# Kernel tuning notes

Measured on AMD Instinct MI355X. Metric: run time of the kernel, lower is better.

The kernel has to match this reference:

```python
import jax, jax.numpy as jnp
import numpy as np

NUM_HEADS = 12
HEAD_DIM = 64
HIDDEN = 768
QMAX = 127.0  # 8-bit symmetric
DOMAIN_MIN, DOMAIN_MAX = -10.0, 0.0
NUM_INTERVALS = 12


def _build_pla_coeffs():
    xs = np.linspace(DOMAIN_MIN, DOMAIN_MAX, 1001)
    ys = np.exp(xs)
    intervals = np.linspace(DOMAIN_MIN, DOMAIN_MAX, NUM_INTERVALS + 1)
    ms, cs = [], []
    for i in range(NUM_INTERVALS):
        a, b = intervals[i], intervals[i + 1]
        mask = (xs >= a) & (xs <= b)
        m, c = np.polyfit(xs[mask], ys[mask], 1)
        ms.append(m)
        cs.append(c)
    return (jnp.asarray(ms, jnp.float32), jnp.asarray(cs, jnp.float32),
            jnp.asarray(intervals, jnp.float32))

COEFFS_M, COEFFS_C, INTERVALS = _build_pla_coeffs()


def quantize(x):
    # per-row (last-dim) abs-max symmetric 8-bit fake quant
    max_val = jnp.max(jnp.abs(x), axis=-1, keepdims=True)
    scale = max_val / QMAX
    scale = jnp.where(scale == 0, 1.0, scale)
    return jnp.clip(jnp.round(x / scale), -QMAX, QMAX) * scale


def to_fixed_point(x, bits=32, frac_bits=26):
    scale = 2.0 ** frac_bits
    lo = -2.0 ** (bits - 1)
    hi = 2.0 ** (bits - 1) - 1
    return jnp.clip(jnp.round(x * scale), lo, hi) / scale


def pla_exp(x):
    xc = jnp.clip(x, DOMAIN_MIN, DOMAIN_MAX)
    # sum(x >= intervals) - 1 == searchsorted(intervals, x, 'right') - 1
    idx = jnp.clip(jnp.searchsorted(INTERVALS, xc, side='right') - 1, 0, NUM_INTERVALS - 1)
    return COEFFS_M[idx] * xc + COEFFS_C[idx]


def pla_softmax(scores):
    shifted = scores - jnp.max(scores, axis=-1, keepdims=True)
    shifted_fx = to_fixed_point(shifted, 32, 26)
    exps = pla_exp(shifted_fx)
    sm = exps / (jnp.sum(exps, axis=-1, keepdims=True) + 1e-9)
    return quantize(sm)


def q_linear(x, W, b):
    # QuantizedLinear: quantize input and weight (per-row), fp bias
    return quantize(x) @ quantize(W).T + b


def split_heads(x):
    B, S, _ = x.shape
    return x.reshape(B, S, NUM_HEADS, HEAD_DIM).transpose(0, 2, 1, 3)  # bhsd


def mhsa(hidden_states, Wq, bq, Wk, bk, Wv, bv, Wo, bo):
    B, S, H = hidden_states.shape
    scale = HEAD_DIM ** -0.5
    q = split_heads(q_linear(hidden_states, Wq, bq))
    k = split_heads(q_linear(hidden_states, Wk, bk))
    v = split_heads(q_linear(hidden_states, Wv, bv))
    # per-row quantization makes tile-wise quant identical to full quant
    scores = jnp.einsum('bhqd,bhkd->bhqk', quantize(q), quantize(k)) * scale
    probs = pla_softmax(scores)
    ctx = jnp.einsum('bhqk,bhkd->bhqd', probs, quantize(v))
    ctx = ctx.transpose(0, 2, 1, 3).reshape(B, S, H)
    return q_linear(ctx, Wo, bo)


def setup_inputs() -> dict:
    key = jax.random.key(0)
    ks = jax.random.split(key, 9)
    B, S = 8, 512
    hs = jax.random.normal(ks[0], (B, S, HIDDEN), dtype=jnp.float32)
    def w(k):
        return jax.random.normal(k, (HIDDEN, HIDDEN), dtype=jnp.float32) * 0.02
    def b(k):
        return jax.random.normal(k, (HIDDEN,), dtype=jnp.float32) * 0.02
    return {
        'hidden_states': hs,
        'Wq': w(ks[1]), 'bq': b(ks[2]),
        'Wk': w(ks[3]), 'bk': b(ks[4]),
        'Wv': w(ks[5]), 'bv': b(ks[6]),
        'Wo': w(ks[7]), 'bo': b(ks[8]),
    }


def reference(hidden_states, Wq, bq, Wk, bk, Wv, bv, Wo, bo):
    return mhsa(hidden_states, Wq, bq, Wk, bk, Wv, bv, Wo, bo)
```

## Files before the change

### kernel.cpp

```cpp
#include <hip/hip_runtime.h>
#include <cmath>

#define R_TOT 4096
#define HID   768
#define NHEAD 12
#define HDIM  64
#define SEQ   512
#define BATCH 8

typedef int   v4i  __attribute__((ext_vector_type(4)));
typedef float v4f  __attribute__((ext_vector_type(4)));
typedef _Float16 half8 __attribute__((ext_vector_type(8)));
typedef _Float16 half4v __attribute__((ext_vector_type(4)));

__device__ __forceinline__ void gl_lds16(const signed char* g, signed char* l) {
  __builtin_amdgcn_global_load_lds(
      (const __attribute__((address_space(1))) void*)g,
      (__attribute__((address_space(3))) void*)l, 16, 0, 0);
}

struct PlaConsts { float m[12]; float c[12]; float b[13]; };

static PlaConsts build_pla() {
  PlaConsts pc;
  const int NPTS = 1001;
  static double xs[NPTS], ys[NPTS];
  const double step = 10.0 / 1000.0;
  for (int j = 0; j < NPTS; ++j) xs[j] = (double)j * step + (-10.0);
  xs[NPTS - 1] = 0.0;
  for (int j = 0; j < NPTS; ++j) ys[j] = std::exp(xs[j]);
  double bnd[13];
  const double step2 = 10.0 / 12.0;
  for (int k = 0; k < 13; ++k) bnd[k] = (double)k * step2 + (-10.0);
  bnd[12] = 0.0;
  for (int i = 0; i < 12; ++i) {
    const double a = bnd[i], bb = bnd[i + 1];
    double sx = 0, sy = 0; int n = 0;
    for (int j = 0; j < NPTS; ++j)
      if (xs[j] >= a && xs[j] <= bb) { sx += xs[j]; sy += ys[j]; ++n; }
    const double xm = sx / n, ym = sy / n;
    double sxx = 0, sxy = 0;
    for (int j = 0; j < NPTS; ++j)
      if (xs[j] >= a && xs[j] <= bb) {
        const double dx = xs[j] - xm;
        sxx += dx * dx; sxy += dx * (ys[j] - ym);
      }
    const double m = sxy / sxx;
    pc.m[i] = (float)m;
    pc.c[i] = (float)(ym - m * xm);
  }
  for (int k = 0; k < 13; ++k) pc.b[k] = (float)bnd[k];
  return pc;
}
static const PlaConsts g_pla = build_pla();

__device__ __forceinline__ void quant_row_wave(const float* __restrict__ x,
                                               signed char* __restrict__ qrow,
                                               float* __restrict__ srow) {
  const int lane = threadIdx.x & 63;
  const float4* x4 = (const float4*)x;
  const float4 a = x4[lane];
  const float4 b = x4[lane + 64];
  const float4 c = x4[lane + 128];
  float m = fmaxf(fmaxf(fabsf(a.x), fabsf(a.y)), fmaxf(fabsf(a.z), fabsf(a.w)));
  m = fmaxf(m, fmaxf(fmaxf(fabsf(b.x), fabsf(b.y)), fmaxf(fabsf(b.z), fabsf(b.w))));
  m = fmaxf(m, fmaxf(fmaxf(fabsf(c.x), fabsf(c.y)), fmaxf(fabsf(c.z), fabsf(c.w))));
  #pragma unroll
  for (int off = 32; off; off >>= 1) m = fmaxf(m, __shfl_xor(m, off));
  float s = m / 127.0f;
  if (s == 0.f) s = 1.f;
  auto qb = [&](float v) -> int {
    return ((int)fminf(fmaxf(rintf(v / s), -127.f), 127.f)) & 255;
  };
  const int p0 = qb(a.x) | (qb(a.y) << 8) | (qb(a.z) << 16) | (qb(a.w) << 24);
  const int p1 = qb(b.x) | (qb(b.y) << 8) | (qb(b.z) << 16) | (qb(b.w) << 24);
  const int p2 = qb(c.x) | (qb(c.y) << 8) | (qb(c.z) << 16) | (qb(c.w) << 24);
  int* q4 = (int*)qrow;
  q4[lane] = p0;
  q4[lane + 64] = p1;
  q4[lane + 128] = p2;
  if (lane == 0) *srow = s;
}

__global__ __launch_bounds__(256)
void quant_rows(const float* __restrict__ src,
                signed char* __restrict__ qout, float* __restrict__ sout) {
  const int row = blockIdx.x * 4 + (threadIdx.x >> 6);
  quant_row_wave(src + (size_t)row * HID, qout + (size_t)row * HID, sout + row);
}

__global__ __launch_bounds__(256)
void quant_all(const float* hs, const float* w0, const float* w1,
               const float* w2, const float* w3,
               signed char* qx, float* sx,
               signed char* q0, signed char* q1, signed char* q2, signed char* q3,
               float* s0, float* s1, float* s2, float* s3) {
  const int row = blockIdx.x * 4 + (threadIdx.x >> 6);
  const float* src; signed char* qo; float* so; int r;
  if (row < R_TOT)             { src = hs; qo = qx; so = sx; r = row; }
  else if (row < R_TOT + 768)  { src = w0; qo = q0; so = s0; r = row - R_TOT; }
  else if (row < R_TOT + 1536) { src = w1; qo = q1; so = s1; r = row - R_TOT - 768; }
  else if (row < R_TOT + 2304) { src = w2; qo = q2; so = s2; r = row - R_TOT - 1536; }
  else                         { src = w3; qo = q3; so = s3; r = row - R_TOT - 2304; }
  quant_row_wave(src + (size_t)r * HID, qo + (size_t)r * HID, so + r);
}

__device__ __forceinline__
void proj_stage(const signed char* __restrict__ qx,
                const signed char* __restrict__ qw,
                int row0, int col0, int k0,
                signed char* __restrict__ Ab, signed char* __restrict__ Bb,
                int w, int lr, int cg) {
  #pragma unroll
  for (int m = 0; m < 4; ++m) {
    const int ci = w * 4 + m;
    gl_lds16(qx + (size_t)(row0 + ci * 8 + lr) * HID + k0 + cg * 16,
             Ab + ci * 1024);
  }
  #pragma unroll
  for (int m = 0; m < 2; ++m) {
    const int ci = w * 2 + m;
    gl_lds16(qw + (size_t)(col0 + ci * 8 + lr) * HID + k0 + cg * 16,
             Bb + ci * 1024);
  }
}

__device__ __forceinline__
void proj_body(int mode,
               const signed char* __restrict__ qx, const float* __restrict__ sx,
               const signed char* __restrict__ qw, const float* __restrict__ sw,
               const float* __restrict__ bias,
               signed char* __restrict__ qo, float* __restrict__ so,
               _Float16* __restrict__ vt, float* __restrict__ fo,
               signed char* Al, signed char* Bl) {
  const int tid = threadIdx.x;
  const int w = tid >> 6, lane = tid & 63;
  const int n = lane & 15, quad = lane >> 4;
  const int row0 = blockIdx.x * 128, col0 = blockIdx.y * 64;
  const int lr = lane >> 3;
  const int lc = lane & 7;
  const int cg = lc ^ lr;
  v4i acc[2][4];
  #pragma unroll
  for (int s = 0; s < 2; ++s)
    #pragma unroll
    for (int j = 0; j < 4; ++j) acc[s][j] = (v4i){0, 0, 0, 0};

  proj_stage(qx, qw, row0, col0, 0, Al, Bl, w, lr, cg);
  __syncthreads();

  #pragma unroll
  for (int it = 0; it < 6; ++it) {
    signed char* Ac = Al + (it & 1) * 16384;
    signed char* Bc = Bl + (it & 1) * 8192;
    if (it < 5)
      proj_stage(qx, qw, row0, col0, (it + 1) * 128,
                 Al + ((it & 1) ^ 1) * 16384, Bl + ((it & 1) ^ 1) * 8192,
                 w, lr, cg);
    #pragma unroll
    for (int ks4 = 0; ks4 < 8; ks4 += 4) {
      const int sw16 = ((quad + ks4) ^ (n & 7)) * 16;
      const v4i af0 = *(const v4i*)&Ac[(w * 16 + n) * 128 + sw16];
      const v4i af1 = *(const v4i*)&Ac[(64 + w * 16 + n) * 128 + sw16];
      #pragma unroll
      for (int j = 0; j < 4; ++j) {
        const v4i bf = *(const v4i*)&Bc[(j * 16 + n) * 128 + sw16];
        acc[0][j] = __builtin_amdgcn_mfma_i32_16x16x64_i8(af0, bf, acc[0][j], 0, 0, 0);
        acc[1][j] = __builtin_amdgcn_mfma_i32_16x16x64_i8(af1, bf, acc[1][j], 0, 0, 0);
      }
    }
    if (it < 5) __syncthreads();
  }

  float swc4[4], bc4[4];
  #pragma unroll
  for (int j = 0; j < 4; ++j) {
    swc4[j] = sw[col0 + j * 16 + n];
    bc4[j] = bias[col0 + j * 16 + n];
  }
  #pragma unroll
  for (int s = 0; s < 2; ++s) {
    const int mrow = s * 64 + w * 16 + quad * 4;
    float sxr[4];
    #pragma unroll
    for (int r = 0; r < 4; ++r) sxr[r] = sx[row0 + mrow + r];
    float vals[4][4];
    #pragma unroll
    for (int j = 0; j < 4; ++j)
      #pragma unroll
      for (int r = 0; r < 4; ++r)
        vals[j][r] = (float)acc[s][j][r] * (sxr[r] * swc4[j]) + bc4[j];
    if (mode == 1) {
      const int h = blockIdx.y;
      #pragma unroll
      for (int r = 0; r < 4; ++r) {
        float m = 0.f;
        #pragma unroll
        for (int j = 0; j < 4; ++j) m = fmaxf(m, fabsf(vals[j][r]));
        #pragma unroll
        for (int off = 1; off < 16; off <<= 1) m = fmaxf(m, __shfl_xor(m, off));
        float sq = m / 127.0f;
        if (sq == 0.f) sq = 1.f;
        const int grow = row0 + mrow + r;
        const int bidx = grow >> 9, sidx = grow & 511;
        const size_t rowidx = ((size_t)bidx * NHEAD + h) * SEQ + sidx;
        #pragma unroll
        for (int j = 0; j < 4; ++j) {
          float q = fminf(fmaxf(rintf(vals[j][r] / sq), -127.f), 127.f);
          qo[rowidx * HDIM + j * 16 + n] = (signed char)(int)q;
        }
        if (n == 0) so[rowidx] = sq;
      }
    } else if (mode == 2) {
      const int h = blockIdx.y;
      float srow[4];
      #pragma unroll
      for (int r = 0; r < 4; ++r) {
        float m = 0.f;
        #pragma unroll
        for (int j = 0; j < 4; ++j) m = fmaxf(m, fabsf(vals[j][r]));
        #pragma unroll
        for (int off = 1; off < 16; off <<= 1) m = fmaxf(m, __shfl_xor(m, off));
        float sq = m / 127.0f;
        if (sq == 0.f) sq = 1.f;
        srow[r] = sq;
      }
      const int grow0 = row0 + mrow;
      const int bidx = grow0 >> 9, sidx = grow0 & 511;
      const int kb = sidx >> 5, ko = sidx & 31;
      const size_t hbv = (size_t)bidx * NHEAD + h;
      #pragma unroll
      for (int j = 0; j < 4; ++j) {
        half4v hv;
        #pragma unroll
        for (int r = 0; r < 4; ++r) {
          float q = fminf(fmaxf(rintf(vals[j][r] / srow[r]), -127.f), 127.f);
          hv[r] = (_Float16)(q * srow[r]);
        }
        *(half4v*)(vt + ((hbv * 16 + kb) * 64 + j * 16 + n) * 32 + ko) = hv;
      }
    } else {
      #pragma unroll
      for (int r = 0; r < 4; ++r) {
        const size_t base = (size_t)(row0 + mrow + r) * HID + col0;
        #pragma unroll
        for (int j = 0; j < 4; ++j)
          fo[base + j * 16 + n] = vals[j][r];
      }
    }
  }
}

__global__ __launch_bounds__(256)
void proj_qkv(const signed char* __restrict__ qx, const float* __restrict__ sx,
              const signed char* qwq, const float* swq, const float* bq,
              signed char* qqd, float* qqs,
              const signed char* qwk, const float* swk, const float* bk,
              signed char* qkd, float* qks,
              const signed char* qwv, const float* swv, const float* bv,
              _Float16* vt2) {
  __shared__ __align__(16) signed char Al[2 * 128 * 128];
  __shared__ __align__(16) signed char Bl[2 * 64 * 128];
  if (blockIdx.z == 0)
    proj_body(1, qx, sx, qwq, swq, bq, qqd, qqs, nullptr, nullptr, Al, Bl);
  else if (blockIdx.z == 1)
    proj_body(1, qx, sx, qwk, swk, bk, qkd, qks, nullptr, nullptr, Al, Bl);
  else
    proj_body(2, qx, sx, qwv, swv, bv, nullptr, nullptr, vt2, nullptr, Al, Bl);
}

__global__ __launch_bounds__(256)
void proj_out(const signed char* __restrict__ qx, const float* __restrict__ sx,
              const signed char* qw, const float* sw, const float* bias,
              float* fo) {
  __shared__ __align__(16) signed char Al[2 * 128 * 128];
  __shared__ __align__(16) signed char Bl[2 * 64 * 128];
  proj_body(0, qx, sx, qw, sw, bias, nullptr, nullptr, nullptr, fo, Al, Bl);
}

__device__ __forceinline__
void softmax_exp_tile(float (&s)[8][4], float mx26, const float4* __restrict__ pt4,
                      float& sum_out, float& amax_out) {
  float sum = 0.f, amax = 0.f;
  #pragma unroll
  for (int t = 0; t < 8; ++t) {
    #pragma unroll
    for (int r = 0; r < 4; ++r) {
      float sh = s[t][r] - mx26;
      sh = fmaxf(sh, -671088640.0f);
      const float tq = rintf(sh);
      const float xc = tq * 1.4901161193847656e-08f;
      int g = (int)((xc + 10.0f) * 1.2f);
      g = g > 11 ? 11 : g;
      float4 E = pt4[g];
      int gn = g + ((xc >= E.y) ? 1 : 0) - ((xc < E.x) ? 1 : 0);
      gn = gn < 0 ? 0 : (gn > 11 ? 11 : gn);
      if (gn != g) E = pt4[gn];
      const float e = __fadd_rn(__fmul_rn(E.z, xc), E.w);
      s[t][r] = e;
      sum += e;
      amax = fmaxf(amax, fabsf(e));
    }
  }
  sum += __shfl_xor(sum, 16);
  sum += __shfl_xor(sum, 32);
  amax = fmaxf(amax, __shfl_xor(amax, 16));
  amax = fmaxf(amax, __shfl_xor(amax, 32));
  sum_out = sum; amax_out = amax;
}

__device__ __forceinline__
void quant_pack_tile(const float (&s)[8][4], float t127,
                     _Float16* __restrict__ phtrow, int w, int quad) {
  #pragma unroll
  for (int t = 0; t < 8; ++t) {
    half4v hq;
    #pragma unroll
    for (int r = 0; r < 4; ++r) {
      const float qf = fminf(fmaxf(rintf(s[t][r] * t127), -127.f), 127.f);
      hq[r] = (_Float16)qf;
    }
    *(half4v*)&phtrow[(t * 4 + w) * 16 + quad * 4] = hq;
  }
}

__device__ __forceinline__
v4f pv_tile(const _Float16* __restrict__ vbase, const _Float16* __restrict__ prow) {
  v4f acc = {0.f, 0.f, 0.f, 0.f};
  #pragma unroll
  for (int kt = 0; kt < 16; ++kt) {
    const half8 bf = *(const half8*)(vbase + kt * 2048);
    acc = __builtin_amdgcn_mfma_f32_16x16x32_f16(*(const half8*)(prow + kt * 32), bf, acc, 0, 0, 0);
  }
  return acc;
}

#define PSTR 520
__global__ __launch_bounds__(256)
void attn_kernel(const signed char* __restrict__ qq, const float* __restrict__ qss,
                 const signed char* __restrict__ qk, const float* __restrict__ kss,
                 const _Float16* __restrict__ vt2,
                 float* __restrict__ ctx, const PlaConsts pc) {
  __shared__ __align__(16) _Float16 PhT[2][16 * PSTR];
  __shared__ __align__(16) float red_max[2][16][4];
  __shared__ __align__(16) float red_sum[2][16][4];
  __shared__ __align__(16) float red_amax[2][16][4];
  __shared__ float psa[2][16];
  __shared__ __align__(16) float4 pt4[12];

  const int tid = threadIdx.x;
  const int q0 = blockIdx.x * 32;
  const int hh = blockIdx.y, bz = blockIdx.z;
  const size_t hb = (size_t)bz * NHEAD + hh;
  const signed char* qqh = qq + (hb * SEQ + q0) * HDIM;
  const signed char* qkh = qk + hb * SEQ * HDIM;
  const float* ksp = kss + hb * SEQ;

  if (tid < 12)
    pt4[tid] = make_float4(pc.b[tid], pc.b[tid + 1], pc.m[tid], pc.c[tid]);

  const int w = tid >> 6, lane = tid & 63;
  const int n = lane & 15, quad = lane >> 4;

  float s26[2][8][4];
  {
    const v4i qf0 = *(const v4i*)(qqh + (size_t)n * HDIM + quad * 16);
    const v4i qf1 = *(const v4i*)(qqh + (size_t)(16 + n) * HDIM + quad * 16);
    const float qs0 = (qss[hb * SEQ + q0 + n] * 0.125f) * 67108864.0f;
    const float qs1 = (qss[hb * SEQ + q0 + 16 + n] * 0.125f) * 67108864.0f;
    float vmax0 = -3.0e38f, vmax1 = -3.0e38f;
    #pragma unroll
    for (int t = 0; t < 8; ++t) {
      const int kc0 = (t * 4 + w) * 16;
      const v4i kfrag = *(const v4i*)(qkh + (size_t)(kc0 + n) * HDIM + quad * 16);
      const float4 ks4 = *(const float4*)(ksp + kc0 + quad * 4);
      v4i zero = {};
      const v4i a0 = __builtin_amdgcn_mfma_i32_16x16x64_i8(kfrag, qf0, zero, 0, 0, 0);
      const v4i a1 = __builtin_amdgcn_mfma_i32_16x16x64_i8(kfrag, qf1, zero, 0, 0, 0);
      const float ks[4] = {ks4.x, ks4.y, ks4.z, ks4.w};
      #pragma unroll
      for (int r = 0; r < 4; ++r) {
        const float v0 = (float)a0[r] * (qs0 * ks[r]);
        const float v1 = (float)a1[r] * (qs1 * ks[r]);
        s26[0][t][r] = v0; vmax0 = fmaxf(vmax0, v0);
        s26[1][t][r] = v1; vmax1 = fmaxf(vmax1, v1);
      }
    }
    vmax0 = fmaxf(vmax0, __shfl_xor(vmax0, 16));
    vmax0 = fmaxf(vmax0, __shfl_xor(vmax0, 32));
    vmax1 = fmaxf(vmax1, __shfl_xor(vmax1, 16));
    vmax1 = fmaxf(vmax1, __shfl_xor(vmax1, 32));
    if (quad == 0) { red_max[0][n][w] = vmax0; red_max[1][n][w] = vmax1; }
  }
  __syncthreads();

  {
    const float4 rm = *(const float4*)&red_max[0][n][0];
    const float mx26 = fmaxf(fmaxf(rm.x, rm.y), fmaxf(rm.z, rm.w));
    float sum, amax;
    softmax_exp_tile(s26[0], mx26, pt4, sum, amax);
    if (quad == 0) { red_sum[0][n][w] = sum; red_amax[0][n][w] = amax; }
  }
  __syncthreads();

  {
    const float4 rs = *(const float4*)&red_sum[0][n][0];
    const float4 ra = *(const float4*)&red_amax[0][n][0];
    float denom = (rs.x + rs.y) + (rs.z + rs.w);
    denom = __fadd_rn(denom, 1e-9f);
    const float rden = 1.0f / denom;
    const float am = fmaxf(fmaxf(ra.x, ra.y), fmaxf(ra.z, ra.w));
    float ps = (am * rden) / 127.0f;
    if (ps == 0.f) ps = 1.f;
    if (w == 0 && quad == 0) psa[0][n] = ps;
    const float t127 = 127.0f / am;
    quant_pack_tile(s26[0], t127, &PhT[0][n * PSTR], w, quad);

    const float4 rm = *(const float4*)&red_max[1][n][0];
    const float mx26 = fmaxf(fmaxf(rm.x, rm.y), fmaxf(rm.z, rm.w));
    float sum, amax;
    softmax_exp_tile(s26[1], mx26, pt4, sum, amax);
    if (quad == 0) { red_sum[1][n][w] = sum; red_amax[1][n][w] = amax; }
  }
  __syncthreads();

  const _Float16* vbase = vt2 + ((size_t)hb * 16 * 64 + (w * 16 + n)) * 32 + quad * 8;

  {
    const v4f acc0 = pv_tile(vbase, &PhT[0][n * PSTR + quad * 8]);

    const float4 rs = *(const float4*)&red_sum[1][n][0];
    const float4 ra = *(const float4*)&red_amax[1][n][0];
    float denom = (rs.x + rs.y) + (rs.z + rs.w);
    denom = __fadd_rn(denom, 1e-9f);
    const float rden = 1.0f / denom;
    const float am = fmaxf(fmaxf(ra.x, ra.y), fmaxf(ra.z, ra.w));
    float ps = (am * rden) / 127.0f;
    if (ps == 0.f) ps = 1.f;
    if (w == 0 && quad == 0) psa[1][n] = ps;
    const float t127 = 127.0f / am;
    quant_pack_tile(s26[1], t127, &PhT[1][n * PSTR], w, quad);

    #pragma unroll
    for (int r = 0; r < 4; ++r) {
      const int row = quad * 4 + r;
      ctx[((size_t)bz * SEQ + q0 + row) * HID + (size_t)hh * HDIM + w * 16 + n] =
          acc0[r] * psa[0][row];
    }
  }
  __syncthreads();

  {
    const v4f acc1 = pv_tile(vbase, &PhT[1][n * PSTR + quad * 8]);
    #pragma unroll
    for (int r = 0; r < 4; ++r) {
      const int row = quad * 4 + r;
      ctx[((size_t)bz * SEQ + q0 + 16 + row) * HID + (size_t)hh * HDIM + w * 16 + n] =
          acc1[r] * psa[1][row];
    }
  }
}

extern "C" void kernel_launch(void* const* d_in, const int* in_sizes, int n_in,
                              void* d_out, int out_size, void* d_ws, size_t ws_size,
                              hipStream_t stream) {
  (void)in_sizes; (void)n_in; (void)out_size; (void)ws_size;
  const float* hs = (const float*)d_in[0];
  const float* Wq = (const float*)d_in[1];
  const float* bq = (const float*)d_in[2];
  const float* Wk = (const float*)d_in[3];
  const float* bk = (const float*)d_in[4];
  const float* Wv = (const float*)d_in[5];
  const float* bv = (const float*)d_in[6];
  const float* Wo = (const float*)d_in[7];
  const float* bo = (const float*)d_in[8];
  float* out = (float*)d_out;

  char* ws = (char*)d_ws;
  size_t off = 0;
  auto alloc = [&](size_t bytes) -> char* {
    char* p = ws + off;
    off += (bytes + 255) & ~(size_t)255;
    return p;
  };
  signed char* qx  = (signed char*)alloc((size_t)R_TOT * HID);
  float*       sx  = (float*)alloc((size_t)R_TOT * 4);
  signed char* qwq = (signed char*)alloc((size_t)HID * HID);
  signed char* qwk = (signed char*)alloc((size_t)HID * HID);
  signed char* qwv = (signed char*)alloc((size_t)HID * HID);
  signed char* qwo = (signed char*)alloc((size_t)HID * HID);
  float*       swq = (float*)alloc((size_t)HID * 4);
  float*       swk = (float*)alloc((size_t)HID * 4);
  float*       swv = (float*)alloc((size_t)HID * 4);
  float*       swo = (float*)alloc((size_t)HID * 4);
  signed char* qqd = (signed char*)alloc((size_t)R_TOT * HID);
  float*       qqs = (float*)alloc((size_t)BATCH * NHEAD * SEQ * 4);
  signed char* qkd = (signed char*)alloc((size_t)R_TOT * HID);
  float*       qks = (float*)alloc((size_t)BATCH * NHEAD * SEQ * 4);
  float*       ctx = (float*)alloc((size_t)R_TOT * HID * 4);
  _Float16*    vt2 = (_Float16*)alloc((size_t)BATCH * NHEAD * HDIM * SEQ * 2);
  signed char* qc  = qx;
  float*       scs = sx;

  quant_all<<<(R_TOT + 4 * HID) / 4, 256, 0, stream>>>(
      hs, Wq, Wk, Wv, Wo, qx, sx,
      qwq, qwk, qwv, qwo, swq, swk, swv, swo);

  proj_qkv<<<dim3(R_TOT / 128, HID / 64, 3), 256, 0, stream>>>(
      qx, sx, qwq, swq, bq, qqd, qqs,
      qwk, swk, bk, qkd, qks,
      qwv, swv, bv, vt2);

  attn_kernel<<<dim3(SEQ / 32, NHEAD, BATCH), 256, 0, stream>>>(
      qqd, qqs, qkd, qks, vt2, ctx, g_pla);

  quant_rows<<<R_TOT / 4, 256, 0, stream>>>(ctx, qc, scs);
  proj_out<<<dim3(R_TOT / 128, HID / 64), 256, 0, stream>>>(
      qc, scs, qwo, swo, bo, out);
}
```

Before: 152.0 us.

## Fuse all pipeline stages into one cooperative persistent kernel with grid syncs

Replaces the five separate kernel launches with one cooperative persistent kernel of 768 blocks. Each stage loops over its former grid's work items and stages are separated by grid-wide barriers, with shared memory reused across stages. This removes launch gaps and per-kernel ramp-up and tail between stages. In exchange it adds grid.sync cost, fixes occupancy at 3 blocks per CU with a 48KB shared buffer, and leaves load imbalance where a stage's work count is not a multiple of the grid size. The old multi-launch path is kept as a fallback if the cooperative launch fails.

```diff
diff --git a/kernel.cpp b/kernel.cpp
--- a/kernel.cpp
+++ b/kernel.cpp
@@ -1,5 +1,8 @@
 #include <hip/hip_runtime.h>
+#include <hip/hip_cooperative_groups.h>
 #include <cmath>
+
+namespace cg = cooperative_groups;
 
 #define R_TOT 4096
 #define HID   768
@@ -7,6 +10,7 @@
 #define HDIM  64
 #define SEQ   512
 #define BATCH 8
+#define GRID_N 768
 
 typedef int   v4i  __attribute__((ext_vector_type(4)));
 typedef float v4f  __attribute__((ext_vector_type(4)));
@@ -82,6 +86,22 @@
   if (lane == 0) *srow = s;
 }
 
+__device__ __forceinline__
+void quant_all_job(int row, const float* hs, const float* w0, const float* w1,
+                   const float* w2, const float* w3,
+                   signed char* qx, float* sx,
+                   signed char* q0, signed char* q1, signed char* q2,
+                   signed char* q3,
+                   float* s0, float* s1, float* s2, float* s3) {
+  const float* src; signed char* qo; float* so; int r;
+  if (row < R_TOT)             { src = hs; qo = qx; so = sx; r = row; }
+  else if (row < R_TOT + 768)  { src = w0; qo = q0; so = s0; r = row - R_TOT; }
+  else if (row < R_TOT + 1536) { src = w1; qo = q1; so = s1; r = row - R_TOT - 768; }
+  else if (row < R_TOT + 2304) { src = w2; qo = q2; so = s2; r = row - R_TOT - 1536; }
+  else                         { src = w3; qo = q3; so = s3; r = row - R_TOT - 2304; }
+  quant_row_wave(src + (size_t)r * HID, qo + (size_t)r * HID, so + r);
+}
+
 __global__ __launch_bounds__(256)
 void quant_rows(const float* __restrict__ src,
                 signed char* __restrict__ qout, float* __restrict__ sout) {
@@ -96,13 +116,7 @@
                signed char* q0, signed char* q1, signed char* q2, signed char* q3,
                float* s0, float* s1, float* s2, float* s3) {
   const int row = blockIdx.x * 4 + (threadIdx.x >> 6);
-  const float* src; signed char* qo; float* so; int r;
-  if (row < R_TOT)             { src = hs; qo = qx; so = sx; r = row; }
-  else if (row < R_TOT + 768)  { src = w0; qo = q0; so = s0; r = row - R_TOT; }
-  else if (row < R_TOT + 1536) { src = w1; qo = q1; so = s1; r = row - R_TOT - 768; }
-  else if (row < R_TOT + 2304) { src = w2; qo = q2; so = s2; r = row - R_TOT - 1536; }
-  else                         { src = w3; qo = q3; so = s3; r = row - R_TOT - 2304; }
-  quant_row_wave(src + (size_t)r * HID, qo + (size_t)r * HID, so + r);
+  quant_all_job(row, hs, w0, w1, w2, w3, qx, sx, q0, q1, q2, q3, s0, s1, s2, s3);
 }
 
 __device__ __forceinline__
@@ -126,7 +140,7 @@
 }
 
 __device__ __forceinline__
-void proj_body(int mode,
+void proj_body(int mode, int bx, int by,
                const signed char* __restrict__ qx, const float* __restrict__ sx,
                const signed char* __restrict__ qw, const float* __restrict__ sw,
                const float* __restrict__ bias,
@@ -136,7 +150,7 @@
   const int tid = threadIdx.x;
   const int w = tid >> 6, lane = tid & 63;
   const int n = lane & 15, quad = lane >> 4;
-  const int row0 = blockIdx.x * 128, col0 = blockIdx.y * 64;
+  const int row0 = bx * 128, col0 = by * 64;
   const int lr = lane >> 3;
   const int lc = lane & 7;
   const int cg = lc ^ lr;
@@ -146,6 +160,7 @@
     #pragma unroll
     for (int j = 0; j < 4; ++j) acc[s][j] = (v4i){0, 0, 0, 0};
 
+  __syncthreads();
   proj_stage(qx, qw, row0, col0, 0, Al, Bl, w, lr, cg);
   __syncthreads();
 
@@ -191,7 +206,7 @@
       for (int r = 0; r < 4; ++r)
         vals[j][r] = (float)acc[s][j][r] * (sxr[r] * swc4[j]) + bc4[j];
     if (mode == 1) {
-      const int h = blockIdx.y;
+      const int h = by;
       #pragma unroll
       for (int r = 0; r < 4; ++r) {
         float m = 0.f;
@@ -212,7 +227,7 @@
         if (n == 0) so[rowidx] = sq;
       }
     } else if (mode == 2) {
-      const int h = blockIdx.y;
+      const int h = by;
       float srow[4];
       #pragma unroll
       for (int r = 0; r < 4; ++r) {
@@ -262,11 +277,11 @@
   __shared__ __align__(16) signed char Al[2 * 128 * 128];
   __shared__ __align__(16) signed char Bl[2 * 64 * 128];
   if (blockIdx.z == 0)
-    proj_body(1, qx, sx, qwq, swq, bq, qqd, qqs, nullptr, nullptr, Al, Bl);
+    proj_body(1, blockIdx.x, blockIdx.y, qx, sx, qwq, swq, bq, qqd, qqs, nullptr, nullptr, Al, Bl);
   else if (blockIdx.z == 1)
-    proj_body(1, qx, sx, qwk, swk, bk, qkd, qks, nullptr, nullptr, Al, Bl);
+    proj_body(1, blockIdx.x, blockIdx.y, qx, sx, qwk, swk, bk, qkd, qks, nullptr, nullptr, Al, Bl);
   else
-    proj_body(2, qx, sx, qwv, swv, bv, nullptr, nullptr, vt2, nullptr, Al, Bl);
+    proj_body(2, blockIdx.x, blockIdx.y, qx, sx, qwv, swv, bv, nullptr, nullptr, vt2, nullptr, Al, Bl);
 }
 
 __global__ __launch_bounds__(256)
@@ -275,7 +290,7 @@
               float* fo) {
   __shared__ __align__(16) signed char Al[2 * 128 * 128];
   __shared__ __align__(16) signed char Bl[2 * 64 * 128];
-  proj_body(0, qx, sx, qw, sw, bias, nullptr, nullptr, nullptr, fo, Al, Bl);
+  proj_body(0, blockIdx.x, blockIdx.y, qx, sx, qw, sw, bias, nullptr, nullptr, nullptr, fo, Al, Bl);
 }
 
 __device__ __forceinline__
@@ -336,28 +351,21 @@
 }
 
 #define PSTR 520
-__global__ __launch_bounds__(256)
-void attn_kernel(const signed char* __restrict__ qq, const float* __restrict__ qss,
-                 const signed char* __restrict__ qk, const float* __restrict__ kss,
-                 const _Float16* __restrict__ vt2,
-                 float* __restrict__ ctx, const PlaConsts pc) {
-  __shared__ __align__(16) _Float16 PhT[2][16 * PSTR];
-  __shared__ __align__(16) float red_max[2][16][4];
-  __shared__ __align__(16) float red_sum[2][16][4];
-  __shared__ __align__(16) float red_amax[2][16][4];
-  __shared__ float psa[2][16];
-  __shared__ __align__(16) float4 pt4[12];
-
+__device__ __forceinline__
+void attn_body(int bxq, int hh, int bz,
+               const signed char* __restrict__ qq, const float* __restrict__ qss,
+               const signed char* __restrict__ qk, const float* __restrict__ kss,
+               const _Float16* __restrict__ vt2, float* __restrict__ ctx,
+               _Float16* __restrict__ PhT0, _Float16* __restrict__ PhT1,
+               float* __restrict__ red_maxp, float* __restrict__ red_sump,
+               float* __restrict__ red_amaxp, float* __restrict__ psap,
+               const float4* __restrict__ pt4) {
   const int tid = threadIdx.x;
-  const int q0 = blockIdx.x * 32;
-  const int hh = blockIdx.y, bz = blockIdx.z;
+  const int q0 = bxq * 32;
   const size_t hb = (size_t)bz * NHEAD + hh;
   const signed char* qqh = qq + (hb * SEQ + q0) * HDIM;
   const signed char* qkh = qk + hb * SEQ * HDIM;
   const float* ksp = kss + hb * SEQ;
-
-  if (tid < 12)
-    pt4[tid] = make_float4(pc.b[tid], pc.b[tid + 1], pc.m[tid], pc.c[tid]);
 
   const int w = tid >> 6, lane = tid & 63;
   const int n = lane & 15, quad = lane >> 4;
@@ -390,74 +398,167 @@
     vmax0 = fmaxf(vmax0, __shfl_xor(vmax0, 32));
     vmax1 = fmaxf(vmax1, __shfl_xor(vmax1, 16));
     vmax1 = fmaxf(vmax1, __shfl_xor(vmax1, 32));
-    if (quad == 0) { red_max[0][n][w] = vmax0; red_max[1][n][w] = vmax1; }
+    if (quad == 0) { red_maxp[n * 4 + w] = vmax0; red_maxp[(16 + n) * 4 + w] = vmax1; }
   }
   __syncthreads();
 
   {
-    const float4 rm = *(const float4*)&red_max[0][n][0];
+    const float4 rm = *(const float4*)(red_maxp + n * 4);
     const float mx26 = fmaxf(fmaxf(rm.x, rm.y), fmaxf(rm.z, rm.w));
     float sum, amax;
     softmax_exp_tile(s26[0], mx26, pt4, sum, amax);
-    if (quad == 0) { red_sum[0][n][w] = sum; red_amax[0][n][w] = amax; }
+    if (quad == 0) { red_sump[n * 4 + w] = sum; red_amaxp[n * 4 + w] = amax; }
   }
   __syncthreads();
 
   {
-    const float4 rs = *(const float4*)&red_sum[0][n][0];
-    const float4 ra = *(const float4*)&red_amax[0][n][0];
+    const float4 rs = *(const float4*)(red_sump + n * 4);
+    const float4 ra = *(const float4*)(red_amaxp + n * 4);
     float denom = (rs.x + rs.y) + (rs.z + rs.w);
     denom = __fadd_rn(denom, 1e-9f);
     const float rden = 1.0f / denom;
     const float am = fmaxf(fmaxf(ra.x, ra.y), fmaxf(ra.z, ra.w));
     float ps = (am * rden) / 127.0f;
     if (ps == 0.f) ps = 1.f;
-    if (w == 0 && quad == 0) psa[0][n] = ps;
+    if (w == 0 && quad == 0) psap[n] = ps;
     const float t127 = 127.0f / am;
-    quant_pack_tile(s26[0], t127, &PhT[0][n * PSTR], w, quad);
-
-    const float4 rm = *(const float4*)&red_max[1][n][0];
+    quant_pack_tile(s26[0], t127, &PhT0[n * PSTR], w, quad);
+
+    const float4 rm = *(const float4*)(red_maxp + (16 + n) * 4);
     const float mx26 = fmaxf(fmaxf(rm.x, rm.y), fmaxf(rm.z, rm.w));
     float sum, amax;
     softmax_exp_tile(s26[1], mx26, pt4, sum, amax);
-    if (quad == 0) { red_sum[1][n][w] = sum; red_amax[1][n][w] = amax; }
+    if (quad == 0) { red_sump[(16 + n) * 4 + w] = sum; red_amaxp[(16 + n) * 4 + w] = amax; }
   }
   __syncthreads();
 
   const _Float16* vbase = vt2 + ((size_t)hb * 16 * 64 + (w * 16 + n)) * 32 + quad * 8;
 
   {
-    const v4f acc0 = pv_tile(vbase, &PhT[0][n * PSTR + quad * 8]);
-
-    const float4 rs = *(const float4*)&red_sum[1][n][0];
-    const float4 ra = *(const float4*)&red_amax[1][n][0];
+    const v4f acc0 = pv_tile(vbase, &PhT0[n * PSTR + quad * 8]);
+
+    const float4 rs = *(const float4*)(red_sump + (16 + n) * 4);
+    const float4 ra = *(const float4*)(red_amaxp + (16 + n) * 4);
     float denom = (rs.x + rs.y) + (rs.z + rs.w);
     denom = __fadd_rn(denom, 1e-9f);
     const float rden = 1.0f / denom;
     const float am = fmaxf(fmaxf(ra.x, ra.y), fmaxf(ra.z, ra.w));
     float ps = (am * rden) / 127.0f;
     if (ps == 0.f) ps = 1.f;
-    if (w == 0 && quad == 0) psa[1][n] = ps;
+    if (w == 0 && quad == 0) psap[16 + n] = ps;
     const float t127 = 127.0f / am;
-    quant_pack_tile(s26[1], t127, &PhT[1][n * PSTR], w, quad);
+    quant_pack_tile(s26[1], t127, &PhT1[n * PSTR], w, quad);
 
     #pragma unroll
     for (int r = 0; r < 4; ++r) {
       const int row = quad * 4 + r;
       ctx[((size_t)bz * SEQ + q0 + row) * HID + (size_t)hh * HDIM + w * 16 + n] =
-          acc0[r] * psa[0][row];
+          acc0[r] * psap[row];
     }
   }
   __syncthreads();
 
   {
-    const v4f acc1 = pv_tile(vbase, &PhT[1][n * PSTR + quad * 8]);
+    const v4f acc1 = pv_tile(vbase, &PhT1[n * PSTR + quad * 8]);
     #pragma unroll
     for (int r = 0; r < 4; ++r) {
       const int row = quad * 4 + r;
       ctx[((size_t)bz * SEQ + q0 + 16 + row) * HID + (size_t)hh * HDIM + w * 16 + n] =
-          acc1[r] * psa[1][row];
-    }
+          acc1[r] * psap[16 + row];
+    }
+  }
+}
+
+__global__ __launch_bounds__(256)
+void attn_kernel(const signed char* __restrict__ qq, const float* __restrict__ qss,
+                 const signed char* __restrict__ qk, const float* __restrict__ kss,
+                 const _Float16* __restrict__ vt2,
+                 float* __restrict__ ctx, const PlaConsts pc) {
+  __shared__ __align__(16) _Float16 PhT[2][16 * PSTR];
+  __shared__ __align__(16) float red_max[2][16][4];
+  __shared__ __align__(16) float red_sum[2][16][4];
+  __shared__ __align__(16) float red_amax[2][16][4];
+  __shared__ __align__(16) float psa[2][16];
+  __shared__ __align__(16) float4 pt4[12];
+  if (threadIdx.x < 12)
+    pt4[threadIdx.x] = make_float4(pc.b[threadIdx.x], pc.b[threadIdx.x + 1],
+                                   pc.m[threadIdx.x], pc.c[threadIdx.x]);
+  attn_body(blockIdx.x, blockIdx.y, blockIdx.z, qq, qss, qk, kss, vt2, ctx,
+            &PhT[0][0], &PhT[1][0], &red_max[0][0][0], &red_sum[0][0][0],
+            &red_amax[0][0][0], &psa[0][0], pt4);
+}
+
+struct MegaArgs {
+  const float *hs, *Wq, *bq, *Wk, *bk, *Wv, *bv, *Wo, *bo;
+  float* out;
+  signed char* qx; float* sx;
+  signed char *qwq, *qwk, *qwv, *qwo;
+  float *swq, *swk, *swv, *swo;
+  signed char* qqd; float* qqs;
+  signed char* qkd; float* qks;
+  float* ctx; _Float16* vt2;
+  PlaConsts pc;
+};
+
+__global__ __launch_bounds__(256, 3)
+void mega_kernel(MegaArgs a) {
+  __shared__ __align__(16) char smem[49152];
+  signed char* Al = (signed char*)smem;
+  signed char* Bl = (signed char*)smem + 32768;
+  cg::grid_group grid = cg::this_grid();
+  const int bid = blockIdx.x;
+  const int wv = threadIdx.x >> 6;
+
+  for (int j = bid; j < 1792; j += GRID_N)
+    quant_all_job(j * 4 + wv, a.hs, a.Wq, a.Wk, a.Wv, a.Wo, a.qx, a.sx,
+                  a.qwq, a.qwk, a.qwv, a.qwo, a.swq, a.swk, a.swv, a.swo);
+  grid.sync();
+
+  for (int j = bid; j < 1152; j += GRID_N) {
+    const int z = j / 384, rem = j - z * 384;
+    const int by = rem >> 5, bx = rem & 31;
+    if (z == 0)
+      proj_body(1, bx, by, a.qx, a.sx, a.qwq, a.swq, a.bq, a.qqd, a.qqs,
+                nullptr, nullptr, Al, Bl);
+    else if (z == 1)
+      proj_body(1, bx, by, a.qx, a.sx, a.qwk, a.swk, a.bk, a.qkd, a.qks,
+                nullptr, nullptr, Al, Bl);
+    else
+      proj_body(2, bx, by, a.qx, a.sx, a.qwv, a.swv, a.bv, nullptr, nullptr,
+                a.vt2, nullptr, Al, Bl);
+  }
+  grid.sync();
+
+  {
+    _Float16* PhT0 = (_Float16*)smem;
+    _Float16* PhT1 = PhT0 + 16 * PSTR;
+    float* red_maxp  = (float*)(smem + 33280);
+    float* red_sump  = (float*)(smem + 33792);
+    float* red_amaxp = (float*)(smem + 34304);
+    float* psap      = (float*)(smem + 34816);
+    float4* pt4      = (float4*)(smem + 34944);
+    if (threadIdx.x < 12)
+      pt4[threadIdx.x] = make_float4(a.pc.b[threadIdx.x], a.pc.b[threadIdx.x + 1],
+                                     a.pc.m[threadIdx.x], a.pc.c[threadIdx.x]);
+    for (int j = bid; j < 1536; j += GRID_N) {
+      const int bx = j & 15, t = j >> 4, by = t % 12, bz = t / 12;
+      attn_body(bx, by, bz, a.qqd, a.qqs, a.qkd, a.qks, a.vt2, a.ctx,
+                PhT0, PhT1, red_maxp, red_sump, red_amaxp, psap, pt4);
+    }
+  }
+  grid.sync();
+
+  for (int j = bid; j < 1024; j += GRID_N) {
+    const int row = j * 4 + wv;
+    quant_row_wave(a.ctx + (size_t)row * HID, a.qx + (size_t)row * HID,
+                   a.sx + row);
+  }
+  grid.sync();
+
+  for (int j = bid; j < 384; j += GRID_N) {
+    const int by = j >> 5, bx = j & 31;
+    proj_body(0, bx, by, a.qx, a.sx, a.qwo, a.swo, a.bo, nullptr, nullptr,
+              nullptr, a.out, Al, Bl);
   }
 }
 
@@ -502,19 +603,33 @@
   signed char* qc  = qx;
   float*       scs = sx;
 
-  quant_all<<<(R_TOT + 4 * HID) / 4, 256, 0, stream>>>(
-      hs, Wq, Wk, Wv, Wo, qx, sx,
-      qwq, qwk, qwv, qwo, swq, swk, swv, swo);
-
-  proj_qkv<<<dim3(R_TOT / 128, HID / 64, 3), 256, 0, stream>>>(
-      qx, sx, qwq, swq, bq, qqd, qqs,
-      qwk, swk, bk, qkd, qks,
-      qwv, swv, bv, vt2);
-
-  attn_kernel<<<dim3(SEQ / 32, NHEAD, BATCH), 256, 0, stream>>>(
-      qqd, qqs, qkd, qks, vt2, ctx, g_pla);
-
-  quant_rows<<<R_TOT / 4, 256, 0, stream>>>(ctx, qc, scs);
-  proj_out<<<dim3(R_TOT / 128, HID / 64), 256, 0, stream>>>(
-      qc, scs, qwo, swo, bo, out);
-}
+  MegaArgs ma;
+  ma.hs = hs; ma.Wq = Wq; ma.bq = bq; ma.Wk = Wk; ma.bk = bk;
+  ma.Wv = Wv; ma.bv = bv; ma.Wo = Wo; ma.bo = bo; ma.out = out;
+  ma.qx = qx; ma.sx = sx;
+  ma.qwq = qwq; ma.qwk = qwk; ma.qwv = qwv; ma.qwo = qwo;
+  ma.swq = swq; ma.swk = swk; ma.swv = swv; ma.swo = swo;
+  ma.qqd = qqd; ma.qqs = qqs; ma.qkd = qkd; ma.qks = qks;
+  ma.ctx = ctx; ma.vt2 = vt2;
+  ma.pc = g_pla;
+
+  void* kargs[] = { (void*)&ma };
+  hipError_t err = hipLaunchCooperativeKernel(
+      reinterpret_cast<const void*>(&mega_kernel),
+      dim3(GRID_N), dim3(256), kargs, 0, stream);
+  if (err != hipSuccess) {
+    (void)hipGetLastError();
+    quant_all<<<(R_TOT + 4 * HID) / 4, 256, 0, stream>>>(
+        hs, Wq, Wk, Wv, Wo, qx, sx,
+        qwq, qwk, qwv, qwo, swq, swk, swv, swo);
+    proj_qkv<<<dim3(R_TOT / 128, HID / 64, 3), 256, 0, stream>>>(
+        qx, sx, qwq, swq, bq, qqd, qqs,
+        qwk, swk, bk, qkd, qks,
+        qwv, swv, bv, vt2);
+    attn_kernel<<<dim3(SEQ / 32, NHEAD, BATCH), 256, 0, stream>>>(
+        qqd, qqs, qkd, qks, vt2, ctx, g_pla);
+    quant_rows<<<R_TOT / 4, 256, 0, stream>>>(ctx, qc, scs);
+    proj_out<<<dim3(R_TOT / 128, HID / 64), 256, 0, stream>>>(
+        qc, scs, qwo, swo, bo, out);
+  }
+}
```

Result: slower. 550.5 us (+262.1%).

## Fuse quantize and projection stages into cooperative persistent kernels with grid sync

Applied to the files above, without the earlier changes.

Replaces the quant_all+proj_qkv pair and the quant_rows+proj_out pair with two cooperative persistent kernels that use grid.sync between the quantization phase and the GEMM phase. This removes launch gaps between dependent kernels but caps the grid at the co-resident block count, adds a grid barrier, and adds a __syncthreads before each proj tile so LDS can be reused across loop iterations. It also splits the softmax PLA lookup table into separate boundary and slope/intercept arrays in LDS, so only one load each is needed per element instead of a conditional second float4 reload. Falls back to the original launches if the cooperative launch fails.

```diff
diff --git a/kernel.cpp b/kernel.cpp
--- a/kernel.cpp
+++ b/kernel.cpp
@@ -1,5 +1,8 @@
 #include <hip/hip_runtime.h>
+#include <hip/hip_cooperative_groups.h>
 #include <cmath>
+
+namespace cg = cooperative_groups;
 
 #define R_TOT 4096
 #define HID   768
@@ -82,6 +85,22 @@
   if (lane == 0) *srow = s;
 }
 
+__device__ __forceinline__
+void quant_all_job(int row, const float* hs, const float* w0, const float* w1,
+                   const float* w2, const float* w3,
+                   signed char* qx, float* sx,
+                   signed char* q0, signed char* q1, signed char* q2,
+                   signed char* q3,
+                   float* s0, float* s1, float* s2, float* s3) {
+  const float* src; signed char* qo; float* so; int r;
+  if (row < R_TOT)             { src = hs; qo = qx; so = sx; r = row; }
+  else if (row < R_TOT + 768)  { src = w0; qo = q0; so = s0; r = row - R_TOT; }
+  else if (row < R_TOT + 1536) { src = w1; qo = q1; so = s1; r = row - R_TOT - 768; }
+  else if (row < R_TOT + 2304) { src = w2; qo = q2; so = s2; r = row - R_TOT - 1536; }
+  else                         { src = w3; qo = q3; so = s3; r = row - R_TOT - 2304; }
+  quant_row_wave(src + (size_t)r * HID, qo + (size_t)r * HID, so + r);
+}
+
 __global__ __launch_bounds__(256)
 void quant_rows(const float* __restrict__ src,
                 signed char* __restrict__ qout, float* __restrict__ sout) {
@@ -96,13 +115,7 @@
                signed char* q0, signed char* q1, signed char* q2, signed char* q3,
                float* s0, float* s1, float* s2, float* s3) {
   const int row = blockIdx.x * 4 + (threadIdx.x >> 6);
-  const float* src; signed char* qo; float* so; int r;
-  if (row < R_TOT)             { src = hs; qo = qx; so = sx; r = row; }
-  else if (row < R_TOT + 768)  { src = w0; qo = q0; so = s0; r = row - R_TOT; }
-  else if (row < R_TOT + 1536) { src = w1; qo = q1; so = s1; r = row - R_TOT - 768; }
-  else if (row < R_TOT + 2304) { src = w2; qo = q2; so = s2; r = row - R_TOT - 1536; }
-  else                         { src = w3; qo = q3; so = s3; r = row - R_TOT - 2304; }
-  quant_row_wave(src + (size_t)r * HID, qo + (size_t)r * HID, so + r);
+  quant_all_job(row, hs, w0, w1, w2, w3, qx, sx, q0, q1, q2, q3, s0, s1, s2, s3);
 }
 
 __device__ __forceinline__
@@ -126,7 +139,7 @@
 }
 
 __device__ __forceinline__
-void proj_body(int mode,
+void proj_body(int mode, int bx, int by,
                const signed char* __restrict__ qx, const float* __restrict__ sx,
                const signed char* __restrict__ qw, const float* __restrict__ sw,
                const float* __restrict__ bias,
@@ -136,7 +149,7 @@
   const int tid = threadIdx.x;
   const int w = tid >> 6, lane = tid & 63;
   const int n = lane & 15, quad = lane >> 4;
-  const int row0 = blockIdx.x * 128, col0 = blockIdx.y * 64;
+  const int row0 = bx * 128, col0 = by * 64;
   const int lr = lane >> 3;
   const int lc = lane & 7;
   const int cg = lc ^ lr;
@@ -146,6 +159,7 @@
     #pragma unroll
     for (int j = 0; j < 4; ++j) acc[s][j] = (v4i){0, 0, 0, 0};
 
+  __syncthreads();
   proj_stage(qx, qw, row0, col0, 0, Al, Bl, w, lr, cg);
   __syncthreads();
 
@@ -191,7 +205,7 @@
       for (int r = 0; r < 4; ++r)
         vals[j][r] = (float)acc[s][j][r] * (sxr[r] * swc4[j]) + bc4[j];
     if (mode == 1) {
-      const int h = blockIdx.y;
+      const int h = by;
       #pragma unroll
       for (int r = 0; r < 4; ++r) {
         float m = 0.f;
@@ -212,7 +226,7 @@
         if (n == 0) so[rowidx] = sq;
       }
     } else if (mode == 2) {
-      const int h = blockIdx.y;
+      const int h = by;
       float srow[4];
       #pragma unroll
       for (int r = 0; r < 4; ++r) {
@@ -262,11 +276,11 @@
   __shared__ __align__(16) signed char Al[2 * 128 * 128];
   __shared__ __align__(16) signed char Bl[2 * 64 * 128];
   if (blockIdx.z == 0)
-    proj_body(1, qx, sx, qwq, swq, bq, qqd, qqs, nullptr, nullptr, Al, Bl);
+    proj_body(1, blockIdx.x, blockIdx.y, qx, sx, qwq, swq, bq, qqd, qqs, nullptr, nullptr, Al, Bl);
   else if (blockIdx.z == 1)
-    proj_body(1, qx, sx, qwk, swk, bk, qkd, qks, nullptr, nullptr, Al, Bl);
+    proj_body(1, blockIdx.x, blockIdx.y, qx, sx, qwk, swk, bk, qkd, qks, nullptr, nullptr, Al, Bl);
   else
-    proj_body(2, qx, sx, qwv, swv, bv, nullptr, nullptr, vt2, nullptr, Al, Bl);
+    proj_body(2, blockIdx.x, blockIdx.y, qx, sx, qwv, swv, bv, nullptr, nullptr, vt2, nullptr, Al, Bl);
 }
 
 __global__ __launch_bounds__(256)
@@ -275,11 +289,79 @@
               float* fo) {
   __shared__ __align__(16) signed char Al[2 * 128 * 128];
   __shared__ __align__(16) signed char Bl[2 * 64 * 128];
-  proj_body(0, qx, sx, qw, sw, bias, nullptr, nullptr, nullptr, fo, Al, Bl);
+  proj_body(0, blockIdx.x, blockIdx.y, qx, sx, qw, sw, bias, nullptr, nullptr, nullptr, fo, Al, Bl);
+}
+
+struct FrontArgs {
+  const float *hs, *Wq, *bq, *Wk, *bk, *Wv, *bv, *Wo;
+  signed char* qx; float* sx;
+  signed char *qwq, *qwk, *qwv, *qwo;
+  float *swq, *swk, *swv, *swo;
+  signed char* qqd; float* qqs;
+  signed char* qkd; float* qks;
+  _Float16* vt2;
+};
+
+__global__ __launch_bounds__(256, 3)
+void fused_front(FrontArgs a) {
+  __shared__ __align__(16) signed char Al[2 * 128 * 128];
+  __shared__ __align__(16) signed char Bl[2 * 64 * 128];
+  cg::grid_group grid = cg::this_grid();
+  const int bid = blockIdx.x;
+  const int wv = threadIdx.x >> 6;
+
+  for (int j = bid; j < 1792; j += 768)
+    quant_all_job(j * 4 + wv, a.hs, a.Wq, a.Wk, a.Wv, a.Wo, a.qx, a.sx,
+                  a.qwq, a.qwk, a.qwv, a.qwo, a.swq, a.swk, a.swv, a.swo);
+  grid.sync();
+
+  for (int j = bid; j < 1152; j += 768) {
+    const int z = j / 384, rem = j - z * 384;
+    const int by = rem >> 5, bx = rem & 31;
+    if (z == 0)
+      proj_body(1, bx, by, a.qx, a.sx, a.qwq, a.swq, a.bq, a.qqd, a.qqs,
+                nullptr, nullptr, Al, Bl);
+    else if (z == 1)
+      proj_body(1, bx, by, a.qx, a.sx, a.qwk, a.swk, a.bk, a.qkd, a.qks,
+                nullptr, nullptr, Al, Bl);
+    else
+      proj_body(2, bx, by, a.qx, a.sx, a.qwv, a.swv, a.bv, nullptr, nullptr,
+                a.vt2, nullptr, Al, Bl);
+  }
+}
+
+struct BackArgs {
+  const float* ctx; signed char* qc; float* scs;
+  const signed char* qwo; const float* swo; const float* bo;
+  float* out;
+};
+
+__global__ __launch_bounds__(256, 2)
+void fused_back(BackArgs a) {
+  __shared__ __align__(16) signed char Al[2 * 128 * 128];
+  __shared__ __align__(16) signed char Bl[2 * 64 * 128];
+  cg::grid_group grid = cg::this_grid();
+  const int bid = blockIdx.x;
+  const int wv = threadIdx.x >> 6;
+
+  for (int j = bid; j < 1024; j += 512) {
+    const int row = j * 4 + wv;
+    quant_row_wave(a.ctx + (size_t)row * HID, a.qc + (size_t)row * HID,
+                   a.scs + row);
+  }
+  grid.sync();
+
+  for (int j = bid; j < 384; j += 512) {
+    const int by = j >> 5, bx = j & 31;
+    proj_body(0, bx, by, a.qc, a.scs, a.qwo, a.swo, a.bo, nullptr, nullptr,
+              nullptr, a.out, Al, Bl);
+  }
 }
 
 __device__ __forceinline__
-void softmax_exp_tile(float (&s)[8][4], float mx26, const float4* __restrict__ pt4,
+void softmax_exp_tile(float (&s)[8][4], float mx26,
+                      const float2* __restrict__ bnd2,
+                      const float2* __restrict__ mc2,
                       float& sum_out, float& amax_out) {
   float sum = 0.f, amax = 0.f;
   #pragma unroll
@@ -292,11 +374,11 @@
       const float xc = tq * 1.4901161193847656e-08f;
       int g = (int)((xc + 10.0f) * 1.2f);
       g = g > 11 ? 11 : g;
-      float4 E = pt4[g];
-      int gn = g + ((xc >= E.y) ? 1 : 0) - ((xc < E.x) ? 1 : 0);
+      const float2 bd = bnd2[g];
+      int gn = g + ((xc >= bd.y) ? 1 : 0) - ((xc < bd.x) ? 1 : 0);
       gn = gn < 0 ? 0 : (gn > 11 ? 11 : gn);
-      if (gn != g) E = pt4[gn];
-      const float e = __fadd_rn(__fmul_rn(E.z, xc), E.w);
+      const float2 mc = mc2[gn];
+      const float e = __fadd_rn(__fmul_rn(mc.x, xc), mc.y);
       s[t][r] = e;
       sum += e;
       amax = fmaxf(amax, fabsf(e));
@@ -345,8 +427,9 @@
   __shared__ __align__(16) float red_max[2][16][4];
   __shared__ __align__(16) float red_sum[2][16][4];
   __shared__ __align__(16) float red_amax[2][16][4];
-  __shared__ float psa[2][16];
-  __shared__ __align__(16) float4 pt4[12];
+  __shared__ __align__(16) float psa[2][16];
+  __shared__ __align__(16) float2 bnd2[12];
+  __shared__ __align__(16) float2 mc2[12];
 
   const int tid = threadIdx.x;
   const int q0 = blockIdx.x * 32;
@@ -356,8 +439,10 @@
   const signed char* qkh = qk + hb * SEQ * HDIM;
   const float* ksp = kss + hb * SEQ;
 
-  if (tid < 12)
-    pt4[tid] = make_float4(pc.b[tid], pc.b[tid + 1], pc.m[tid], pc.c[tid]);
+  if (tid < 12) {
+    bnd2[tid] = make_float2(pc.b[tid], pc.b[tid + 1]);
+    mc2[tid] = make_float2(pc.m[tid], pc.c[tid]);
+  }
 
   const int w = tid >> 6, lane = tid & 63;
   const int n = lane & 15, quad = lane >> 4;
@@ -398,7 +483,7 @@
     const float4 rm = *(const float4*)&red_max[0][n][0];
     const float mx26 = fmaxf(fmaxf(rm.x, rm.y), fmaxf(rm.z, rm.w));
     float sum, amax;
-    softmax_exp_tile(s26[0], mx26, pt4, sum, amax);
+    softmax_exp_tile(s26[0], mx26, bnd2, mc2, sum, amax);
     if (quad == 0) { red_sum[0][n][w] = sum; red_amax[0][n][w] = amax; }
   }
   __syncthreads();
@@ -419,7 +504,7 @@
     const float4 rm = *(const float4*)&red_max[1][n][0];
     const float mx26 = fmaxf(fmaxf(rm.x, rm.y), fmaxf(rm.z, rm.w));
     float sum, amax;
-    softmax_exp_tile(s26[1], mx26, pt4, sum, amax);
+    softmax_exp_tile(s26[1], mx26, bnd2, mc2, sum, amax);
     if (quad == 0) { red_sum[1][n][w] = sum; red_amax[1][n][w] = amax; }
   }
   __syncthreads();
@@ -502,19 +587,45 @@
   signed char* qc  = qx;
   float*       scs = sx;
 
-  quant_all<<<(R_TOT + 4 * HID) / 4, 256, 0, stream>>>(
-      hs, Wq, Wk, Wv, Wo, qx, sx,
-      qwq, qwk, qwv, qwo, swq, swk, swv, swo);
-
-  proj_qkv<<<dim3(R_TOT / 128, HID / 64, 3), 256, 0, stream>>>(
-      qx, sx, qwq, swq, bq, qqd, qqs,
-      qwk, swk, bk, qkd, qks,
-      qwv, swv, bv, vt2);
+  FrontArgs fa;
+  fa.hs = hs; fa.Wq = Wq; fa.bq = bq; fa.Wk = Wk; fa.bk = bk;
+  fa.Wv = Wv; fa.bv = bv; fa.Wo = Wo;
+  fa.qx = qx; fa.sx = sx;
+  fa.qwq = qwq; fa.qwk = qwk; fa.qwv = qwv; fa.qwo = qwo;
+  fa.swq = swq; fa.swk = swk; fa.swv = swv; fa.swo = swo;
+  fa.qqd = qqd; fa.qqs = qqs; fa.qkd = qkd; fa.qks = qks;
+  fa.vt2 = vt2;
+
+  void* fargs[] = { (void*)&fa };
+  hipError_t e1 = hipLaunchCooperativeKernel(
+      reinterpret_cast<const void*>(&fused_front),
+      dim3(768), dim3(256), fargs, 0, stream);
+  if (e1 != hipSuccess) {
+    (void)hipGetLastError();
+    quant_all<<<(R_TOT + 4 * HID) / 4, 256, 0, stream>>>(
+        hs, Wq, Wk, Wv, Wo, qx, sx,
+        qwq, qwk, qwv, qwo, swq, swk, swv, swo);
+    proj_qkv<<<dim3(R_TOT / 128, HID / 64, 3), 256, 0, stream>>>(
+        qx, sx, qwq, swq, bq, qqd, qqs,
+        qwk, swk, bk, qkd, qks,
+        qwv, swv, bv, vt2);
+  }
 
   attn_kernel<<<dim3(SEQ / 32, NHEAD, BATCH), 256, 0, stream>>>(
       qqd, qqs, qkd, qks, vt2, ctx, g_pla);
 
-  quant_rows<<<R_TOT / 4, 256, 0, stream>>>(ctx, qc, scs);
-  proj_out<<<dim3(R_TOT / 128, HID / 64), 256, 0, stream>>>(
-      qc, scs, qwo, swo, bo, out);
-}
+  BackArgs ba;
+  ba.ctx = ctx; ba.qc = qc; ba.scs = scs;
+  ba.qwo = qwo; ba.swo = swo; ba.bo = bo; ba.out = out;
+
+  void* bargs[] = { (void*)&ba };
+  hipError_t e2 = hipLaunchCooperativeKernel(
+      reinterpret_cast<const void*>(&fused_back),
+      dim3(512), dim3(256), bargs, 0, stream);
+  if (e2 != hipSuccess) {
+    (void)hipGetLastError();
+    quant_rows<<<R_TOT / 4, 256, 0, stream>>>(ctx, qc, scs);
+    proj_out<<<dim3(R_TOT / 128, HID / 64), 256, 0, stream>>>(
+        qc, scs, qwo, swo, bo, out);
+  }
+}
```

Result: slower. 331.2 us (+117.9%).
